# Kernel optimization log

Hardware: AMD Instinct MI355X
Metric: run time of the kernel (lower is better)

The kernel has to match this reference:

```python
import jax, jax.numpy as jnp
import numpy as np

B, L, D, H = 2, 4096, 512, 8
HD = D // H  # head_dim = 64


def setup_inputs() -> dict:
    key = jax.random.key(0)
    ks = jax.random.split(key, 5)
    s = 0.02
    return {
        "x": jax.random.normal(ks[0], (B, L, D), dtype=jnp.float32),
        "w_qkv": jax.random.normal(ks[1], (D, 3 * D), dtype=jnp.float32) * s,
        "b_qkv": jax.random.normal(ks[2], (3 * D,), dtype=jnp.float32) * s,
        "w_o": jax.random.normal(ks[3], (D, D), dtype=jnp.float32) * s,
        "b_o": jax.random.normal(ks[4], (D,), dtype=jnp.float32) * s,
    }


def reference(x, w_qkv, b_qkv, w_o, b_o):
    b, l, _ = x.shape
    # QKV projection, then split heads: [B, L, 3D] -> [B, H, L, 3*HD]
    qkv = x @ w_qkv + b_qkv
    qkv = qkv.reshape(b, l, H, 3 * HD).transpose(0, 2, 1, 3)
    q, k, v = jnp.split(qkv, 3, axis=-1)  # each [B, H, L, HD]
    scale = 1.0 / jnp.sqrt(jnp.asarray(HD, dtype=q.dtype))
    # full score matrix [B, H, L, L], softmax in float32 (matches .float() cast)
    scores = jnp.einsum('bhld,bhsd->bhls', q, k) * scale
    attn = jax.nn.softmax(scores.astype(jnp.float32), axis=-1).astype(q.dtype)
    values = jnp.einsum('bhls,bhsd->bhld', attn, v)  # [B, H, L, HD]
    values = values.transpose(0, 2, 1, 3).reshape(b, l, D)
    return values @ w_o + b_o
```

## Files before the change

### kernel.cpp

```cpp
#include <hip/hip_runtime.h>


#define B_  2
#define L_  4096
#define D_  512
#define H_  8
#define HD_ 64
#define BH_ (B_*H_)
#define M_  (B_*L_)
#define QKVN (3*D_)
#define HEADSZ (BH_*L_*HD_)

typedef unsigned short ushort;
typedef unsigned int uint;
typedef __bf16 bf16x8 __attribute__((ext_vector_type(8)));
typedef float  f32x4  __attribute__((ext_vector_type(4)));
typedef float  f32x16 __attribute__((ext_vector_type(16)));

typedef const __attribute__((address_space(1))) void g_void;
typedef __attribute__((address_space(3))) void l_void;

#define C2_ 0.18033688011112042f

__device__ __forceinline__ ushort f2bf(float f) {
    __bf16 h = (__bf16)f;
    return __builtin_bit_cast(ushort, h);
}

__device__ __forceinline__ uint pack2(float lo, float hi) {
    return (uint)f2bf(lo) | ((uint)f2bf(hi) << 16);
}

__global__ __launch_bounds__(256)
void prep_k(const float* __restrict__ x, ushort* __restrict__ xb,
            const float* __restrict__ wq, ushort* __restrict__ wtq,
            const float* __restrict__ wo, ushort* __restrict__ wto)
{
    int bid = blockIdx.x, tid = threadIdx.x;
    if (bid < 4096) {
        int idx = bid * 256 + tid;
        float4 v = ((const float4*)x)[idx];
        ushort4 o; o.x = f2bf(v.x); o.y = f2bf(v.y); o.z = f2bf(v.z); o.w = f2bf(v.w);
        ((ushort4*)xb)[idx] = o;
    } else if (bid < 7168) {
        int idx = (bid - 4096) * 256 + tid;
        int c = idx / D_, r = idx % D_;
        wtq[idx] = f2bf(wq[r * QKVN + c]);
    } else {
        int idx = (bid - 7168) * 256 + tid;
        int c = idx / D_, r = idx % D_;
        wto[idx] = f2bf(wo[r * D_ + c]);
    }
}

#define TP 66
__global__ __launch_bounds__(256)
void transpose_v(const ushort* __restrict__ V, ushort* __restrict__ VT) {
    __shared__ ushort T[64 * TP];
    const int tid = threadIdx.x;
    const int bh = blockIdx.y;
    const int l0 = blockIdx.x * 64;
    const int base = bh * (L_ * HD_);
    #pragma unroll
    for (int i = 0; i < 2; i++) {
        int c = i * 256 + tid;
        int l = c >> 3, dc = (c & 7) * 8;
        uint4 v = *(const uint4*)&V[base + (l0 + l) * HD_ + dc];
        uint* p = (uint*)&T[l * TP + dc];
        p[0] = v.x; p[1] = v.y; p[2] = v.z; p[3] = v.w;
    }
    __syncthreads();
    #pragma unroll
    for (int p = 0; p < 2; p++) {
        int c = p * 256 + tid;
        int d = c >> 3, lb = c & 7;
        ushort tmp[8];
        #pragma unroll
        for (int j = 0; j < 8; j++) tmp[j] = T[(lb * 8 + j) * TP + d];
        *(uint4*)&VT[base + d * L_ + l0 + lb * 8] = *(uint4*)tmp;
    }
}

__global__ __launch_bounds__(256)
void gemm_bt(const ushort* __restrict__ A, const ushort* __restrict__ Bt,
             const float* __restrict__ bias, void* __restrict__ out,
             int M, int N, int K, int mode)
{
    __shared__ ushort As[128 * 32];
    __shared__ ushort Bs[128 * 32];

    const int tid  = threadIdx.x;
    const int lane = tid & 63;
    const int wid  = tid >> 6;
    const int wm   = wid >> 1, wn = wid & 1;
    const int lr   = lane & 15;
    const int quad = lane >> 4;
    const int tm = blockIdx.x, tn = blockIdx.y;

    f32x4 acc[4][4] = {};
    const int arow = tm * 128;
    const int brow = tn * 128;

    for (int k0 = 0; k0 < K; k0 += 32) {
        #pragma unroll
        for (int i = 0; i < 2; i++) {
            int c   = i * 256 + tid;
            int row = c >> 2;
            int kk  = (c & 3) * 8;
            __builtin_amdgcn_global_load_lds(
                (g_void*)&A[(size_t)(arow + row) * K + k0 + kk],
                (l_void*)&As[c * 8], 16, 0, 0);
            __builtin_amdgcn_global_load_lds(
                (g_void*)&Bt[(size_t)(brow + row) * K + k0 + kk],
                (l_void*)&Bs[c * 8], 16, 0, 0);
        }
        __syncthreads();

        bf16x8 af[4], bfr[4];
        #pragma unroll
        for (int t = 0; t < 4; t++) {
            af [t] = *(const bf16x8*)&As[(wm * 64 + t * 16 + lr) * 32 + quad * 8];
            bfr[t] = *(const bf16x8*)&Bs[(wn * 64 + t * 16 + lr) * 32 + quad * 8];
        }
        #pragma unroll
        for (int mt = 0; mt < 4; mt++)
            #pragma unroll
            for (int nt = 0; nt < 4; nt++)
                acc[mt][nt] = __builtin_amdgcn_mfma_f32_16x16x32_bf16(
                    af[mt], bfr[nt], acc[mt][nt], 0, 0, 0);
        __syncthreads();
    }

    #pragma unroll
    for (int nt = 0; nt < 4; nt++) {
        int col = tn * 128 + wn * 64 + nt * 16 + lr;
        float bv = bias[col];
        #pragma unroll
        for (int mt = 0; mt < 4; mt++) {
            #pragma unroll
            for (int r = 0; r < 4; r++) {
                int row = tm * 128 + wm * 64 + mt * 16 + quad * 4 + r;
                float v = acc[mt][nt][r] + bv;
                if (mode == 0) {
                    ((float*)out)[(size_t)row * N + col] = v;
                } else {
                    int d = col & 63;
                    int g = col >> 6;
                    int which = g % 3;
                    int h = g / 3;
                    int b = row >> 12;
                    int l = row & (L_ - 1);
                    if (which == 0) v *= C2_;
                    ((ushort*)out)[which * HEADSZ + (((b * H_ + h) * L_ + l) * HD_) + d]
                        = f2bf(v);
                }
            }
        }
    }
}

__global__ __launch_bounds__(256)
void attn_k(const ushort* __restrict__ Q, const ushort* __restrict__ K,
            const ushort* __restrict__ VT, ushort* __restrict__ O)
{
    __shared__ __align__(16) ushort Ksm[2][64 * 64];
    __shared__ __align__(16) ushort Vsm[4][64 * 64];
    __shared__ float Linv[4][32];

    const int tid  = threadIdx.x;
    const int lane = tid & 63;
    const int wid  = tid >> 6;
    const int l31  = lane & 31;
    const int hi   = lane >> 5;

    const int wg  = blockIdx.x;
    const int xcd = wg & 7, sl = wg >> 3;
    const int bh  = (xcd << 1) | (sl >> 5);
    const int q0  = (sl & 31) * 128;
    const size_t base = (size_t)bh * (L_ * HD_);

    const int sr0 = tid >> 3,        sr1 = (tid + 256) >> 3;
    const int sc0 = ((tid & 7) ^ (sr0 & 7)) * 8;
    const int sc1 = ((tid & 7) ^ (sr1 & 7)) * 8;
    const ushort* Kg0 = K  + base + sr0 * HD_ + sc0;
    const ushort* Kg1 = K  + base + sr1 * HD_ + sc1;
    const ushort* Vg0 = VT + base + (size_t)sr0 * L_ + sc0;
    const ushort* Vg1 = VT + base + (size_t)sr1 * L_ + sc1;

    bf16x8 qf[4];
    {
        const ushort* qp = Q + base + (size_t)(q0 + wid * 32 + l31) * HD_ + hi * 8;
        #pragma unroll
        for (int ks = 0; ks < 4; ks++) qf[ks] = *(const bf16x8*)(qp + ks * 16);
    }

    const int swz = (l31 & 7) << 4;
    int cbe[4];
    #pragma unroll
    for (int ks = 0; ks < 4; ks++) cbe[ks] = ((ks * 32 + hi * 16) ^ swz) >> 1;
    const int kr0 = l31 * 64, kr1 = (32 + l31) * 64;

    f32x16 o0 = {}, o1 = {};
    f32x16 sEA, sEB, sOA, sOB;
    float l4[4] = {0.f, 0.f, 0.f, 0.f};

    auto STAGE = [&](int tt) {
        const size_t ko = (size_t)tt * 64 * HD_;
        const int    vo = tt * 64;
        ushort* kb = &Ksm[tt & 1][0];
        ushort* vb = &Vsm[tt & 3][0];
        __builtin_amdgcn_global_load_lds((g_void*)(Kg0 + ko), (l_void*)(kb + tid * 8),        16, 0, 0);
        __builtin_amdgcn_global_load_lds((g_void*)(Kg1 + ko), (l_void*)(kb + tid * 8 + 2048), 16, 0, 0);
        __builtin_amdgcn_global_load_lds((g_void*)(Vg0 + vo), (l_void*)(vb + tid * 8),        16, 0, 0);
        __builtin_amdgcn_global_load_lds((g_void*)(Vg1 + vo), (l_void*)(vb + tid * 8 + 2048), 16, 0, 0);
    };

    auto QK = [&](int tt, f32x16& SA, f32x16& SB) {
        const ushort* kb = &Ksm[tt & 1][0];
        SA = f32x16{}; SB = f32x16{};
        #pragma unroll
        for (int ks = 0; ks < 4; ks++) {
            bf16x8 k0 = *(const bf16x8*)&kb[kr0 + cbe[ks]];
            bf16x8 k1 = *(const bf16x8*)&kb[kr1 + cbe[ks]];
            SA = __builtin_amdgcn_mfma_f32_32x32x16_bf16(k0, qf[ks], SA, 0, 0, 0);
            SB = __builtin_amdgcn_mfma_f32_32x32x16_bf16(k1, qf[ks], SB, 0, 0, 0);
        }
    };

    auto SMPV = [&](int tp, f32x16& SA, f32x16& SB) {
        const ushort* vb = &Vsm[tp & 3][0];
        #pragma unroll
        for (int i = 0; i < 16; i++) { SA[i] = exp2f(SA[i]); SB[i] = exp2f(SB[i]); }
        #pragma unroll
        for (int i = 0; i < 16; i++) l4[i & 3] += SA[i] + SB[i];
        #pragma unroll
        for (int ks = 0; ks < 4; ks++) {
            const f32x16& P = (ks >> 1) ? SB : SA;
            const int r0 = 8 * (ks & 1);
            uint a0 = pack2(P[r0 + 0], P[r0 + 1]);
            uint a1 = pack2(P[r0 + 2], P[r0 + 3]);
            uint b0 = pack2(P[r0 + 4], P[r0 + 5]);
            uint b1 = pack2(P[r0 + 6], P[r0 + 7]);
            asm("v_permlane32_swap_b32 %0, %1" : "+v"(a0), "+v"(b0));
            asm("v_permlane32_swap_b32 %0, %1" : "+v"(a1), "+v"(b1));
            uint4 w; w.x = a0; w.y = a1; w.z = b0; w.w = b1;
            bf16x8 pa = __builtin_bit_cast(bf16x8, w);
            bf16x8 v0 = *(const bf16x8*)&vb[kr0 + cbe[ks]];
            bf16x8 v1 = *(const bf16x8*)&vb[kr1 + cbe[ks]];
            o0 = __builtin_amdgcn_mfma_f32_32x32x16_bf16(pa, v0, o0, 0, 0, 0);
            o1 = __builtin_amdgcn_mfma_f32_32x32x16_bf16(pa, v1, o1, 0, 0, 0);
        }
    };

    STAGE(0);

    for (int t = 0; t < L_ / 64; t += 2) {
        __syncthreads();
        STAGE(t + 1);
        QK(t, sEA, sEB);
        if (t > 0) SMPV(t - 1, sOA, sOB);
        __syncthreads();
        if (t + 2 < L_ / 64) STAGE(t + 2);
        QK(t + 1, sOA, sOB);
        SMPV(t, sEA, sEB);
    }
    SMPV(L_ / 64 - 1, sOA, sOB);

    float lp = (l4[0] + l4[1]) + (l4[2] + l4[3]);
    lp += __shfl_xor(lp, 32, 64);
    if (hi == 0) Linv[wid][l31] = 1.0f / lp;

    const int b = bh >> 3, h = bh & 7;
    #pragma unroll
    for (int r = 0; r < 16; r++) {
        const int qrl = (r & 3) + 8 * (r >> 2) + 4 * hi;
        const float inv = Linv[wid][qrl];
        const size_t row = (size_t)(b * L_ + q0 + wid * 32 + qrl) * D_ + h * HD_ + l31;
        O[row]      = f2bf(o0[r] * inv);
        O[row + 32] = f2bf(o1[r] * inv);
    }
}

extern "C" void kernel_launch(void* const* d_in, const int* in_sizes, int n_in,
                              void* d_out, int out_size, void* d_ws, size_t ws_size,
                              hipStream_t stream)
{
    const float* x     = (const float*)d_in[0];
    const float* w_qkv = (const float*)d_in[1];
    const float* b_qkv = (const float*)d_in[2];
    const float* w_o   = (const float*)d_in[3];
    const float* b_o   = (const float*)d_in[4];

    char* ws = (char*)d_ws;
    size_t o = 0;
    ushort* xb   = (ushort*)(ws + o); o += (size_t)M_ * D_ * 2;
    ushort* qkv  = (ushort*)(ws + o); o += (size_t)3 * HEADSZ * 2;
    ushort* attn = (ushort*)(ws + o); o += (size_t)M_ * D_ * 2;
    ushort* wtq  = (ushort*)(ws + o); o += (size_t)QKVN * D_ * 2;
    ushort* wto  = (ushort*)(ws + o);
    ushort* vt   = xb;

    hipLaunchKernelGGL(prep_k, dim3(8192), dim3(256), 0, stream,
                       x, xb, w_qkv, wtq, w_o, wto);
    hipLaunchKernelGGL(gemm_bt, dim3(M_ / 128, QKVN / 128), dim3(256), 0, stream,
                       xb, wtq, b_qkv, (void*)qkv, M_, QKVN, D_, 1);
    hipLaunchKernelGGL(transpose_v, dim3(L_ / 64, BH_), dim3(256), 0, stream,
                       qkv + 2 * HEADSZ, vt);
    hipLaunchKernelGGL(attn_k, dim3(512), dim3(256), 0, stream,
                       qkv, qkv + HEADSZ, vt, attn);
    hipLaunchKernelGGL(gemm_bt, dim3(M_ / 128, D_ / 128), dim3(256), 0, stream,
                       attn, wto, b_o, d_out, M_, D_, D_, 0);
}
```

Before: 236.0 us.

## Deepen K/V LDS ring buffers to one barrier per tile pair, add MFMA priority

The K shared-memory buffer grows from two to four slots, and the main loop is restructured to process two 64-key tiles per iteration. Each iteration now has a single barrier and prefetches the next two K and V tiles, instead of two barriers per pair. This is meant to cut synchronisation stalls and give the async global-to-LDS loads more time in flight. s_setprio is raised around the MFMA sections so waves doing matrix work get issue priority. The Linv scratch now aliases the K buffer after a final barrier, offsetting the larger LDS footprint, which may reduce occupancy.

```diff
diff --git a/kernel.cpp b/kernel.cpp
--- a/kernel.cpp
+++ b/kernel.cpp
@@ -163,9 +163,8 @@
 void attn_k(const ushort* __restrict__ Q, const ushort* __restrict__ K,
             const ushort* __restrict__ VT, ushort* __restrict__ O)
 {
-    __shared__ __align__(16) ushort Ksm[2][64 * 64];
+    __shared__ __align__(16) ushort Ksm[4][64 * 64];
     __shared__ __align__(16) ushort Vsm[4][64 * 64];
-    __shared__ float Linv[4][32];
 
     const int tid  = threadIdx.x;
     const int lane = tid & 63;
@@ -204,20 +203,23 @@
     f32x16 sEA, sEB, sOA, sOB;
     float l4[4] = {0.f, 0.f, 0.f, 0.f};
 
-    auto STAGE = [&](int tt) {
+    auto STAGE_K = [&](int tt) {
+        ushort* kb = &Ksm[tt & 3][0];
         const size_t ko = (size_t)tt * 64 * HD_;
-        const int    vo = tt * 64;
-        ushort* kb = &Ksm[tt & 1][0];
-        ushort* vb = &Vsm[tt & 3][0];
         __builtin_amdgcn_global_load_lds((g_void*)(Kg0 + ko), (l_void*)(kb + tid * 8),        16, 0, 0);
         __builtin_amdgcn_global_load_lds((g_void*)(Kg1 + ko), (l_void*)(kb + tid * 8 + 2048), 16, 0, 0);
+    };
+    auto STAGE_V = [&](int tt) {
+        ushort* vb = &Vsm[tt & 3][0];
+        const int vo = tt * 64;
         __builtin_amdgcn_global_load_lds((g_void*)(Vg0 + vo), (l_void*)(vb + tid * 8),        16, 0, 0);
         __builtin_amdgcn_global_load_lds((g_void*)(Vg1 + vo), (l_void*)(vb + tid * 8 + 2048), 16, 0, 0);
     };
 
     auto QK = [&](int tt, f32x16& SA, f32x16& SB) {
-        const ushort* kb = &Ksm[tt & 1][0];
+        const ushort* kb = &Ksm[tt & 3][0];
         SA = f32x16{}; SB = f32x16{};
+        __builtin_amdgcn_s_setprio(1);
         #pragma unroll
         for (int ks = 0; ks < 4; ks++) {
             bf16x8 k0 = *(const bf16x8*)&kb[kr0 + cbe[ks]];
@@ -225,6 +227,7 @@
             SA = __builtin_amdgcn_mfma_f32_32x32x16_bf16(k0, qf[ks], SA, 0, 0, 0);
             SB = __builtin_amdgcn_mfma_f32_32x32x16_bf16(k1, qf[ks], SB, 0, 0, 0);
         }
+        __builtin_amdgcn_s_setprio(0);
     };
 
     auto SMPV = [&](int tp, f32x16& SA, f32x16& SB) {
@@ -233,6 +236,7 @@
         for (int i = 0; i < 16; i++) { SA[i] = exp2f(SA[i]); SB[i] = exp2f(SB[i]); }
         #pragma unroll
         for (int i = 0; i < 16; i++) l4[i & 3] += SA[i] + SB[i];
+        __builtin_amdgcn_s_setprio(1);
         #pragma unroll
         for (int ks = 0; ks < 4; ks++) {
             const f32x16& P = (ks >> 1) ? SB : SA;
@@ -250,31 +254,36 @@
             o0 = __builtin_amdgcn_mfma_f32_32x32x16_bf16(pa, v0, o0, 0, 0, 0);
             o1 = __builtin_amdgcn_mfma_f32_32x32x16_bf16(pa, v1, o1, 0, 0, 0);
         }
+        __builtin_amdgcn_s_setprio(0);
     };
 
-    STAGE(0);
-
-    for (int t = 0; t < L_ / 64; t += 2) {
+    STAGE_K(0); STAGE_K(1); STAGE_V(0);
+
+    for (int p = 0; p < L_ / 128; p++) {
+        const int s0 = 2 * p, s1 = s0 + 1;
         __syncthreads();
-        STAGE(t + 1);
-        QK(t, sEA, sEB);
-        if (t > 0) SMPV(t - 1, sOA, sOB);
-        __syncthreads();
-        if (t + 2 < L_ / 64) STAGE(t + 2);
-        QK(t + 1, sOA, sOB);
-        SMPV(t, sEA, sEB);
-    }
+        if (s0 + 2 < L_ / 64) STAGE_K(s0 + 2);
+        if (s0 + 3 < L_ / 64) STAGE_K(s0 + 3);
+        STAGE_V(s1);
+        if (s1 + 1 < L_ / 64) STAGE_V(s1 + 1);
+        QK(s0, sEA, sEB);
+        if (p > 0) SMPV(s0 - 1, sOA, sOB);
+        QK(s1, sOA, sOB);
+        SMPV(s0, sEA, sEB);
+    }
+    __syncthreads();
     SMPV(L_ / 64 - 1, sOA, sOB);
 
+    float* Linv = (float*)&Ksm[0][0];
     float lp = (l4[0] + l4[1]) + (l4[2] + l4[3]);
     lp += __shfl_xor(lp, 32, 64);
-    if (hi == 0) Linv[wid][l31] = 1.0f / lp;
+    if (hi == 0) Linv[wid * 32 + l31] = 1.0f / lp;
 
     const int b = bh >> 3, h = bh & 7;
     #pragma unroll
     for (int r = 0; r < 16; r++) {
         const int qrl = (r & 3) + 8 * (r >> 2) + 4 * hi;
-        const float inv = Linv[wid][qrl];
+        const float inv = Linv[wid * 32 + qrl];
         const size_t row = (size_t)(b * L_ + q0 + wid * 32 + qrl) * D_ + h * HD_ + l31;
         O[row]      = f2bf(o0[r] * inv);
         O[row + 32] = f2bf(o1[r] * inv);
```

After: 238.6 us. Within noise of the previous version (+1.1%).
